# Optimization experiments

Hardware: AMD Instinct MI355X
Metric: run time of the kernel (lower is better)

Reference implementation:

```python
import jax, jax.numpy as jnp
import numpy as np

N = 50000
F_IN = 256
H1, D1 = 8, 8            # conv1: 8 heads x 8 dims, concat -> 64
H2, C = 8, 16            # conv2: 8 heads x num_classes, concat -> 128
NEG_SLOPE = 0.2


def setup_inputs() -> dict:
    key = jax.random.key(0)
    ks = jax.random.split(key, 10)
    x = jax.random.normal(ks[0], (N, F_IN), dtype=jnp.float32)
    edge_index = jax.random.randint(ks[1], (2, 800000), 0, N, dtype=jnp.int64)
    s1 = 1.0 / np.sqrt(F_IN)
    s2 = 1.0 / np.sqrt(H1 * D1)
    return {
        "x": x,
        "edge_index": edge_index,
        "W1": jax.random.normal(ks[2], (F_IN, H1 * D1), dtype=jnp.float32) * s1,
        "a1_src": jax.random.normal(ks[3], (H1, D1), dtype=jnp.float32) * s2,
        "a1_dst": jax.random.normal(ks[4], (H1, D1), dtype=jnp.float32) * s2,
        "b1": jnp.zeros((H1 * D1,), dtype=jnp.float32),
        "W2": jax.random.normal(ks[5], (H1 * D1, H2 * C), dtype=jnp.float32) * s2,
        "a2_src": jax.random.normal(ks[6], (H2, C), dtype=jnp.float32) * (1.0 / np.sqrt(C)),
        "a2_dst": jax.random.normal(ks[7], (H2, C), dtype=jnp.float32) * (1.0 / np.sqrt(C)),
        "b2": jnp.zeros((H2 * C,), dtype=jnp.float32),
    }


def _add_self_loops(edge_index, n):
    loops = jnp.arange(n, dtype=edge_index.dtype)
    return jnp.concatenate([edge_index, jnp.stack([loops, loops])], axis=1)


def _gat_conv(x, src, dst, W, a_src, a_dst, b, heads, out_dim, n):
    # xw: [N, H, O]
    xw = (x @ W).reshape(n, heads, out_dim)
    al_src = jnp.einsum("nho,ho->nh", xw, a_src)  # [N, H]
    al_dst = jnp.einsum("nho,ho->nh", xw, a_dst)
    e = jax.nn.leaky_relu(al_src[src] + al_dst[dst], NEG_SLOPE)  # [E, H]
    # segment softmax over edges sharing a destination node
    e_max = jax.ops.segment_max(e, dst, num_segments=n)
    e_exp = jnp.exp(e - e_max[dst])
    denom = jax.ops.segment_sum(e_exp, dst, num_segments=n)
    alpha = e_exp / (denom[dst] + 1e-16)                          # [E, H]
    msg = xw[src] * alpha[:, :, None]                              # [E, H, O]
    out = jax.ops.segment_sum(msg, dst, num_segments=n)           # [N, H, O]
    return out.reshape(n, heads * out_dim) + b, alpha


def reference(x, edge_index, W1, a1_src, a1_dst, b1, W2, a2_src, a2_dst, b2):
    ei = _add_self_loops(edge_index, N)
    src, dst = ei[0], ei[1]
    # dropout is a no-op at inference (training=False)
    h1, alpha1 = _gat_conv(x, src, dst, W1, a1_src, a1_dst, b1, H1, D1, N)
    h1 = jax.nn.elu(h1)
    h2, _ = _gat_conv(h1, src, dst, W2, a2_src, a2_dst, b2, H2, C, N)
    logp = jax.nn.log_softmax(h2, axis=1)
    return logp, alpha1
```

## Files before the change

### kernel.cpp

```cpp
#include <hip/hip_runtime.h>

#define N_NODES 50000
#define N_EDGES 800000
#define N_TOT   850000
#define NEG 0.2f
#define ELLW 64

#define G1_TILES 391
#define G2_TILES 782

#define NBIN   250
#define NPBIN  200
#define BKBLK  200
#define EPBK   4000
#define BCAP   32
#define OCAP   4096

__device__ __forceinline__ float leaky(float x) { return x > 0.f ? x : NEG * x; }

__device__ __forceinline__ unsigned bf16pk(float a, float b) {
  unsigned ua = __float_as_uint(a), ub = __float_as_uint(b);
  ua = (ua + 0x7FFFu + ((ua >> 16) & 1u)) >> 16;
  ub = (ub + 0x7FFFu + ((ub >> 16) & 1u)) >> 16;
  return ua | (ub << 16);
}
__device__ __forceinline__ float blo(unsigned u) { return __uint_as_float(u << 16); }
__device__ __forceinline__ float bhi(unsigned u) { return __uint_as_float(u & 0xFFFF0000u); }
__device__ __forceinline__ float bh2f(unsigned short h) { return __uint_as_float(((unsigned)h) << 16); }

__global__ __launch_bounds__(256) void bin_gemm1_k(const float* __restrict__ x,
    const float* __restrict__ W1, const float* __restrict__ a1sv, const float* __restrict__ a1dv,
    unsigned short* __restrict__ xw1h, float* __restrict__ al1s, float* __restrict__ a1dd,
    const int* __restrict__ srcA, const int* __restrict__ dstA,
    unsigned* __restrict__ slots, unsigned short* __restrict__ bcnt2,
    unsigned* __restrict__ ofl, int* __restrict__ ofc)
{
  __shared__ __align__(16) char smem[33024];
  const int t = threadIdx.x;
  if (blockIdx.x < BKBLK) {
    unsigned (*buf)[BCAP] = (unsigned(*)[BCAP])smem;
    int* bc = (int*)(smem + 32000);
    for (int k = t; k < NBIN; k += 256) bc[k] = 0;
    __syncthreads();
    const int e0 = blockIdx.x * EPBK;
#pragma unroll
    for (int j = 0; j < 4; ++j) {
      int i4 = j * 256 + t;
      if (i4 < EPBK / 4) {
        int4 s4 = ((const int4*)(srcA + e0))[i4];
        int4 d4 = ((const int4*)(dstA + e0))[i4];
        int dd[4] = {d4.x, d4.y, d4.z, d4.w};
        int ss[4] = {s4.x, s4.y, s4.z, s4.w};
#pragma unroll
        for (int q = 0; q < 4; ++q) {
          int bin = dd[q] / NPBIN;
          unsigned rec = (unsigned)dd[q] | ((unsigned)ss[q] << 16);
          int p = atomicAdd(&bc[bin], 1);
          if (p < BCAP) buf[bin][p] = rec;
          else { int g = atomicAdd(ofc, 1); if (g < OCAP) ofl[g] = rec; }
        }
      }
    }
    __syncthreads();
    const int wv = t >> 6, ln = t & 63;
    for (int b = wv; b < NBIN; b += 4) {
      int c = bc[b]; if (c > BCAP) c = BCAP;
      if (ln == 0) bcnt2[(size_t)b * BKBLK + blockIdx.x] = (unsigned short)c;
      if (ln < c) slots[((size_t)b * BKBLK + blockIdx.x) * BCAP + ln] = buf[b][ln];
    }
    return;
  }
  float* xs  = (float*)smem;
  float* wsm = (float*)(smem + 16384);
  const int tx = t & 15, ty = t >> 4;
  const int n0 = (blockIdx.x - BKBLK) * 128;
  const int nl = t >> 1;
  const int ks = (t & 1) * 16;
  const int wk = t >> 3;
  const int wc = (t & 7) * 8;
  int gn = n0 + nl; if (gn >= N_NODES) gn = N_NODES - 1;
  const float* xrowb = x + (size_t)gn * 256 + ks;

  float acc[8][4];
#pragma unroll
  for (int r = 0; r < 8; ++r)
#pragma unroll
    for (int i = 0; i < 4; ++i) acc[r][i] = 0.f;

  float4 xv0, xv1, xv2, xv3, wv0, wv1;
  {
    const float4* xp = (const float4*)xrowb;
    xv0 = xp[0]; xv1 = xp[1]; xv2 = xp[2]; xv3 = xp[3];
    const float* wrow = W1 + (size_t)wk * 64 + wc;
    wv0 = ((const float4*)wrow)[0];
    wv1 = ((const float4*)wrow)[1];
  }
  for (int kc = 0; kc < 8; ++kc) {
    __syncthreads();
    xs[(ks + 0) * 128 + nl] = xv0.x;  xs[(ks + 1) * 128 + nl] = xv0.y;
    xs[(ks + 2) * 128 + nl] = xv0.z;  xs[(ks + 3) * 128 + nl] = xv0.w;
    xs[(ks + 4) * 128 + nl] = xv1.x;  xs[(ks + 5) * 128 + nl] = xv1.y;
    xs[(ks + 6) * 128 + nl] = xv1.z;  xs[(ks + 7) * 128 + nl] = xv1.w;
    xs[(ks + 8) * 128 + nl] = xv2.x;  xs[(ks + 9) * 128 + nl] = xv2.y;
    xs[(ks + 10) * 128 + nl] = xv2.z; xs[(ks + 11) * 128 + nl] = xv2.w;
    xs[(ks + 12) * 128 + nl] = xv3.x; xs[(ks + 13) * 128 + nl] = xv3.y;
    xs[(ks + 14) * 128 + nl] = xv3.z; xs[(ks + 15) * 128 + nl] = xv3.w;
    ((float4*)&wsm[wk * 64 + wc])[0] = wv0;
    ((float4*)&wsm[wk * 64 + wc])[1] = wv1;
    __syncthreads();
    if (kc < 7) {
      const int kb = (kc + 1) * 32;
      const float4* xp = (const float4*)(xrowb + kb);
      xv0 = xp[0]; xv1 = xp[1]; xv2 = xp[2]; xv3 = xp[3];
      const float* wrow = W1 + (size_t)(kb + wk) * 64 + wc;
      wv0 = ((const float4*)wrow)[0];
      wv1 = ((const float4*)wrow)[1];
    }
#pragma unroll 4
    for (int k = 0; k < 32; ++k) {
      float4 xa = *(const float4*)&xs[k * 128 + ty * 8];
      float4 xb = *(const float4*)&xs[k * 128 + ty * 8 + 4];
      float4 wv = *(const float4*)&wsm[k * 64 + tx * 4];
      float xn[8]; *(float4*)&xn[0] = xa; *(float4*)&xn[4] = xb;
      float wn[4]; *(float4*)wn = wv;
#pragma unroll
      for (int r = 0; r < 8; ++r)
#pragma unroll
        for (int i = 0; i < 4; ++i) acc[r][i] += xn[r] * wn[i];
    }
  }
  float cs[4], cd[4];
#pragma unroll
  for (int i = 0; i < 4; ++i) { cs[i] = a1sv[tx * 4 + i]; cd[i] = a1dv[tx * 4 + i]; }
#pragma unroll
  for (int r = 0; r < 8; ++r) {
    int n = n0 + ty * 8 + r;
    if (n >= N_NODES) break;
    uint2 pk;
    pk.x = bf16pk(acc[r][0], acc[r][1]);
    pk.y = bf16pk(acc[r][2], acc[r][3]);
    *(uint2*)(xw1h + (size_t)n * 64 + tx * 4) = pk;
    float ps = acc[r][0] * cs[0] + acc[r][1] * cs[1] + acc[r][2] * cs[2] + acc[r][3] * cs[3];
    float pd = acc[r][0] * cd[0] + acc[r][1] * cd[1] + acc[r][2] * cd[2] + acc[r][3] * cd[3];
    ps += __shfl_xor(ps, 1);
    pd += __shfl_xor(pd, 1);
    if ((tx & 1) == 0) {
      al1s[n * 8 + (tx >> 1)] = ps;
      a1dd[n * 16 + (tx >> 1)] = pd;
    }
  }
}

__global__ __launch_bounds__(256) void ell_k(const unsigned* __restrict__ slots,
    const unsigned short* __restrict__ bcnt2, const unsigned* __restrict__ ofl,
    const int* __restrict__ ofc, int* __restrict__ cnt, unsigned short* __restrict__ ell)
{
  __shared__ unsigned short ell_lds[NPBIN * ELLW];
  __shared__ int cnt_lds[NPBIN];
  const int t = threadIdx.x;
  const int b = blockIdx.x;
  for (int k = t; k < NPBIN; k += 256) cnt_lds[k] = 0;
  __syncthreads();
  if (t < BKBLK) {
    int c = bcnt2[(size_t)b * BKBLK + t];
    const uint4* sp4 = (const uint4*)(slots + ((size_t)b * BKBLK + t) * BCAP);
    uint4 R[8];
#pragma unroll
    for (int q = 0; q < 8; ++q) R[q] = sp4[q];
#pragma unroll
    for (int j = 0; j < BCAP; ++j) {
      if (j < c) {
        unsigned rec = ((const unsigned*)R)[j];
        int row = (int)(rec & 0xFFFFu) - b * NPBIN;
        int p = atomicAdd(&cnt_lds[row], 1);
        if (p < ELLW) ell_lds[row * ELLW + p] = (unsigned short)(rec >> 16);
      }
    }
  }
  __syncthreads();
  int oc = *ofc; if (oc > OCAP) oc = OCAP;
  for (int i = t; i < oc; i += 256) {
    unsigned rec = ofl[i];
    int d = rec & 0xFFFFu;
    if (d >= b * NPBIN && d < (b + 1) * NPBIN) {
      int p = atomicAdd(&cnt_lds[d - b * NPBIN], 1);
      if (p < ELLW) ell_lds[(d - b * NPBIN) * ELLW + p] = (unsigned short)(rec >> 16);
    }
  }
  __syncthreads();
  const uint4* s4 = (const uint4*)ell_lds;
  uint4* d4 = (uint4*)(ell + (size_t)b * NPBIN * ELLW);
  for (int i = t; i < NPBIN * ELLW / 8; i += 256) d4[i] = s4[i];
  for (int k = t; k < NPBIN; k += 256) cnt[b * NPBIN + k] = cnt_lds[k];
}

__global__ __launch_bounds__(256) void agg1_k(const unsigned short* __restrict__ xw1h,
    const float* __restrict__ al1s, float* __restrict__ a1dd,
    const int* __restrict__ cnt, const unsigned short* __restrict__ ell,
    const float* __restrict__ b1, float* __restrict__ h1)
{
  const int lane = threadIdx.x & 63;
  const int n = blockIdx.x * 4 + (threadIdx.x >> 6);
  if (n >= N_NODES) return;
  const int h = lane >> 3;
  const float ad = a1dd[n * 16 + h];
  float ws = __expf(leaky(al1s[n * 8 + h] + ad));
  float den0 = ws, den1r = 0.f;
  float acc0 = ws * bh2f(xw1h[(size_t)n * 64 + lane]), acc1 = 0.f;
  int num = cnt[n]; if (num > ELLW) num = ELLW;
  const uint4* cp = (const uint4*)(ell + (size_t)n * ELLW);
  int i = 0;
  for (; i + 8 <= num; i += 8) {
    uint4 A = cp[i >> 3];
    int s0 = A.x & 0xFFFF, s1 = (int)(A.x >> 16);
    int s2 = A.y & 0xFFFF, s3 = (int)(A.y >> 16);
    int s4 = A.z & 0xFFFF, s5 = (int)(A.z >> 16);
    int s6 = A.w & 0xFFFF, s7 = (int)(A.w >> 16);
    float l0 = al1s[s0 * 8 + h] + ad, l1 = al1s[s1 * 8 + h] + ad;
    float l2 = al1s[s2 * 8 + h] + ad, l3 = al1s[s3 * 8 + h] + ad;
    float l4 = al1s[s4 * 8 + h] + ad, l5 = al1s[s5 * 8 + h] + ad;
    float l6 = al1s[s6 * 8 + h] + ad, l7 = al1s[s7 * 8 + h] + ad;
    float v0 = bh2f(xw1h[(size_t)s0 * 64 + lane]), v1 = bh2f(xw1h[(size_t)s1 * 64 + lane]);
    float v2 = bh2f(xw1h[(size_t)s2 * 64 + lane]), v3 = bh2f(xw1h[(size_t)s3 * 64 + lane]);
    float v4 = bh2f(xw1h[(size_t)s4 * 64 + lane]), v5 = bh2f(xw1h[(size_t)s5 * 64 + lane]);
    float v6 = bh2f(xw1h[(size_t)s6 * 64 + lane]), v7 = bh2f(xw1h[(size_t)s7 * 64 + lane]);
    float w0 = __expf(leaky(l0)), w1 = __expf(leaky(l1));
    float w2 = __expf(leaky(l2)), w3 = __expf(leaky(l3));
    float w4 = __expf(leaky(l4)), w5 = __expf(leaky(l5));
    float w6 = __expf(leaky(l6)), w7 = __expf(leaky(l7));
    acc0 += w0 * v0; acc1 += w1 * v1; acc0 += w2 * v2; acc1 += w3 * v3;
    acc0 += w4 * v4; acc1 += w5 * v5; acc0 += w6 * v6; acc1 += w7 * v7;
    den0 += w0 + w2 + w4 + w6; den1r += w1 + w3 + w5 + w7;
  }
  for (; i + 4 <= num; i += 4) {
    uint2 A = *(const uint2*)(ell + (size_t)n * ELLW + i);
    int s0 = A.x & 0xFFFF, s1 = (int)(A.x >> 16);
    int s2 = A.y & 0xFFFF, s3 = (int)(A.y >> 16);
    float l0 = al1s[s0 * 8 + h] + ad, l1 = al1s[s1 * 8 + h] + ad;
    float l2 = al1s[s2 * 8 + h] + ad, l3 = al1s[s3 * 8 + h] + ad;
    float v0 = bh2f(xw1h[(size_t)s0 * 64 + lane]), v1 = bh2f(xw1h[(size_t)s1 * 64 + lane]);
    float v2 = bh2f(xw1h[(size_t)s2 * 64 + lane]), v3 = bh2f(xw1h[(size_t)s3 * 64 + lane]);
    float w0 = __expf(leaky(l0)), w1 = __expf(leaky(l1));
    float w2 = __expf(leaky(l2)), w3 = __expf(leaky(l3));
    acc0 += w0 * v0; acc1 += w1 * v1; acc0 += w2 * v2; acc1 += w3 * v3;
    den0 += w0 + w2; den1r += w1 + w3;
  }
  for (; i < num; ++i) {
    int s = ell[(size_t)n * ELLW + i];
    float w = __expf(leaky(al1s[s * 8 + h] + ad));
    acc0 += w * bh2f(xw1h[(size_t)s * 64 + lane]);
    den0 += w;
  }
  float den = den0 + den1r, acc = acc0 + acc1;
  if ((lane & 7) == 0) a1dd[n * 16 + 8 + h] = den;
  float o = acc / (den + 1e-16f) + b1[lane];
  h1[(size_t)n * 64 + lane] = o > 0.f ? o : (__expf(o) - 1.f);
}

__global__ __launch_bounds__(256) void gemm2_alpha_k(const float* __restrict__ h1,
    const float* __restrict__ W2, const float* __restrict__ a2sv, const float* __restrict__ a2dv,
    unsigned* __restrict__ xw2b, float* __restrict__ al2s, float* __restrict__ al2d,
    const int* __restrict__ srcA, const int* __restrict__ dstA,
    const float* __restrict__ al1s, const float* __restrict__ a1dd,
    float* __restrict__ alpha_out)
{
  __shared__ float xs[64 * 64];
  __shared__ float wsm[64 * 128];
  if (blockIdx.x >= G2_TILES) {
    int e = (blockIdx.x - G2_TILES) * 256 + threadIdx.x;
    if (e >= N_TOT) return;
    int s, d;
    if (e < N_EDGES) { s = srcA[e]; d = dstA[e]; }
    else             { s = d = e - N_EDGES; }
    float4 as0 = ((const float4*)(al1s + s * 8))[0];
    float4 as1 = ((const float4*)(al1s + s * 8))[1];
    const float4* dd = (const float4*)(a1dd + d * 16);
    float4 ad0 = dd[0];
    float4 ad1 = dd[1];
    float4 dn0 = dd[2];
    float4 dn1 = dd[3];
    float4 o0, o1;
    o0.x = __expf(leaky(as0.x + ad0.x)) / (dn0.x + 1e-16f);
    o0.y = __expf(leaky(as0.y + ad0.y)) / (dn0.y + 1e-16f);
    o0.z = __expf(leaky(as0.z + ad0.z)) / (dn0.z + 1e-16f);
    o0.w = __expf(leaky(as0.w + ad0.w)) / (dn0.w + 1e-16f);
    o1.x = __expf(leaky(as1.x + ad1.x)) / (dn1.x + 1e-16f);
    o1.y = __expf(leaky(as1.y + ad1.y)) / (dn1.y + 1e-16f);
    o1.z = __expf(leaky(as1.z + ad1.z)) / (dn1.z + 1e-16f);
    o1.w = __expf(leaky(as1.w + ad1.w)) / (dn1.w + 1e-16f);
    ((float4*)(alpha_out + (size_t)e * 8))[0] = o0;
    ((float4*)(alpha_out + (size_t)e * 8))[1] = o1;
    return;
  }
  const int t = threadIdx.x;
  const int tx = t & 15, ty = t >> 4;
  const int n0 = blockIdx.x * 64;
  {
    const int nl = t >> 2;
    const int ks = (t & 3) * 16;
    int gn = n0 + nl; if (gn >= N_NODES) gn = N_NODES - 1;
    const float4* hp = (const float4*)(h1 + (size_t)gn * 64 + ks);
#pragma unroll
    for (int j = 0; j < 4; ++j) {
      float4 v = hp[j];
      xs[(ks + 4 * j + 0) * 64 + nl] = v.x;
      xs[(ks + 4 * j + 1) * 64 + nl] = v.y;
      xs[(ks + 4 * j + 2) * 64 + nl] = v.z;
      xs[(ks + 4 * j + 3) * 64 + nl] = v.w;
    }
    const int wk = t >> 2;
    const int wc = (t & 3) * 32;
    const float4* wp = (const float4*)(W2 + (size_t)wk * 128 + wc);
    float4* wd = (float4*)&wsm[wk * 128 + wc];
#pragma unroll
    for (int j = 0; j < 8; ++j) wd[j] = wp[j];
  }
  __syncthreads();
  float acc[4][8];
#pragma unroll
  for (int r = 0; r < 4; ++r)
#pragma unroll
    for (int i = 0; i < 8; ++i) acc[r][i] = 0.f;
#pragma unroll 4
  for (int k = 0; k < 64; ++k) {
    float4 xa = *(const float4*)&xs[k * 64 + ty * 4];
    float4 wa = *(const float4*)&wsm[k * 128 + tx * 8];
    float4 wb = *(const float4*)&wsm[k * 128 + tx * 8 + 4];
    float xn[4]; *(float4*)xn = xa;
    float wn[8]; *(float4*)&wn[0] = wa; *(float4*)&wn[4] = wb;
#pragma unroll
    for (int r = 0; r < 4; ++r)
#pragma unroll
      for (int i = 0; i < 8; ++i) acc[r][i] += xn[r] * wn[i];
  }
  float cs[8], cd[8];
#pragma unroll
  for (int i = 0; i < 8; ++i) { cs[i] = a2sv[tx * 8 + i]; cd[i] = a2dv[tx * 8 + i]; }
#pragma unroll
  for (int r = 0; r < 4; ++r) {
    int n = n0 + ty * 4 + r;
    if (n >= N_NODES) break;
    uint4 pk;
    pk.x = bf16pk(acc[r][0], acc[r][1]);
    pk.y = bf16pk(acc[r][2], acc[r][3]);
    pk.z = bf16pk(acc[r][4], acc[r][5]);
    pk.w = bf16pk(acc[r][6], acc[r][7]);
    *(uint4*)(xw2b + (size_t)n * 64 + tx * 4) = pk;
    float ps = 0.f, pd = 0.f;
#pragma unroll
    for (int i = 0; i < 8; ++i) { ps += acc[r][i] * cs[i]; pd += acc[r][i] * cd[i]; }
    ps += __shfl_xor(ps, 1);
    pd += __shfl_xor(pd, 1);
    if ((tx & 1) == 0) {
      al2s[n * 8 + (tx >> 1)] = ps;
      al2d[n * 8 + (tx >> 1)] = pd;
    }
  }
}

__global__ __launch_bounds__(256) void agg2_k(const unsigned* __restrict__ xw2b,
    const float* __restrict__ al2s, const float* __restrict__ al2d,
    const int* __restrict__ cnt, const unsigned short* __restrict__ ell,
    const float* __restrict__ b2, float* __restrict__ logp)
{
  const int lane = threadIdx.x & 63;
  const int n = blockIdx.x * 4 + (threadIdx.x >> 6);
  if (n >= N_NODES) return;
  const int h = lane >> 3;
  const float ad = al2d[n * 8 + h];
  float ws = __expf(leaky(al2s[n * 8 + h] + ad));
  unsigned su = xw2b[(size_t)n * 64 + lane];
  float den0 = ws, den1r = 0.f;
  float ax0 = ws * blo(su), ay0 = ws * bhi(su), ax1 = 0.f, ay1 = 0.f;
  int num = cnt[n]; if (num > ELLW) num = ELLW;
  const uint4* cp = (const uint4*)(ell + (size_t)n * ELLW);
  int i = 0;
  for (; i + 8 <= num; i += 8) {
    uint4 A = cp[i >> 3];
    int s0 = A.x & 0xFFFF, s1 = (int)(A.x >> 16);
    int s2 = A.y & 0xFFFF, s3 = (int)(A.y >> 16);
    int s4 = A.z & 0xFFFF, s5 = (int)(A.z >> 16);
    int s6 = A.w & 0xFFFF, s7 = (int)(A.w >> 16);
    float l0 = al2s[s0 * 8 + h] + ad, l1 = al2s[s1 * 8 + h] + ad;
    float l2 = al2s[s2 * 8 + h] + ad, l3 = al2s[s3 * 8 + h] + ad;
    float l4 = al2s[s4 * 8 + h] + ad, l5 = al2s[s5 * 8 + h] + ad;
    float l6 = al2s[s6 * 8 + h] + ad, l7 = al2s[s7 * 8 + h] + ad;
    unsigned u0 = xw2b[(size_t)s0 * 64 + lane], u1 = xw2b[(size_t)s1 * 64 + lane];
    unsigned u2 = xw2b[(size_t)s2 * 64 + lane], u3 = xw2b[(size_t)s3 * 64 + lane];
    unsigned u4 = xw2b[(size_t)s4 * 64 + lane], u5 = xw2b[(size_t)s5 * 64 + lane];
    unsigned u6 = xw2b[(size_t)s6 * 64 + lane], u7 = xw2b[(size_t)s7 * 64 + lane];
    float w0 = __expf(leaky(l0)), w1 = __expf(leaky(l1));
    float w2 = __expf(leaky(l2)), w3 = __expf(leaky(l3));
    float w4 = __expf(leaky(l4)), w5 = __expf(leaky(l5));
    float w6 = __expf(leaky(l6)), w7 = __expf(leaky(l7));
    ax0 += w0 * blo(u0); ay0 += w0 * bhi(u0);
    ax1 += w1 * blo(u1); ay1 += w1 * bhi(u1);
    ax0 += w2 * blo(u2); ay0 += w2 * bhi(u2);
    ax1 += w3 * blo(u3); ay1 += w3 * bhi(u3);
    ax0 += w4 * blo(u4); ay0 += w4 * bhi(u4);
    ax1 += w5 * blo(u5); ay1 += w5 * bhi(u5);
    ax0 += w6 * blo(u6); ay0 += w6 * bhi(u6);
    ax1 += w7 * blo(u7); ay1 += w7 * bhi(u7);
    den0 += w0 + w2 + w4 + w6; den1r += w1 + w3 + w5 + w7;
  }
  for (; i + 4 <= num; i += 4) {
    uint2 A = *(const uint2*)(ell + (size_t)n * ELLW + i);
    int s0 = A.x & 0xFFFF, s1 = (int)(A.x >> 16);
    int s2 = A.y & 0xFFFF, s3 = (int)(A.y >> 16);
    float l0 = al2s[s0 * 8 + h] + ad, l1 = al2s[s1 * 8 + h] + ad;
    float l2 = al2s[s2 * 8 + h] + ad, l3 = al2s[s3 * 8 + h] + ad;
    unsigned u0 = xw2b[(size_t)s0 * 64 + lane], u1 = xw2b[(size_t)s1 * 64 + lane];
    unsigned u2 = xw2b[(size_t)s2 * 64 + lane], u3 = xw2b[(size_t)s3 * 64 + lane];
    float w0 = __expf(leaky(l0)), w1 = __expf(leaky(l1));
    float w2 = __expf(leaky(l2)), w3 = __expf(leaky(l3));
    ax0 += w0 * blo(u0); ay0 += w0 * bhi(u0);
    ax1 += w1 * blo(u1); ay1 += w1 * bhi(u1);
    ax0 += w2 * blo(u2); ay0 += w2 * bhi(u2);
    ax1 += w3 * blo(u3); ay1 += w3 * bhi(u3);
    den0 += w0 + w2; den1r += w1 + w3;
  }
  for (; i < num; ++i) {
    int s = ell[(size_t)n * ELLW + i];
    float w = __expf(leaky(al2s[s * 8 + h] + ad));
    unsigned u = xw2b[(size_t)s * 64 + lane];
    ax0 += w * blo(u); ay0 += w * bhi(u); den0 += w;
  }
  float inv = 1.f / (den0 + den1r + 1e-16f);
  float o0 = (ax0 + ax1) * inv + b2[2 * lane];
  float o1 = (ay0 + ay1) * inv + b2[2 * lane + 1];
  float mx = fmaxf(o0, o1);
#pragma unroll
  for (int off = 1; off < 64; off <<= 1) mx = fmaxf(mx, __shfl_xor(mx, off));
  float se = __expf(o0 - mx) + __expf(o1 - mx);
#pragma unroll
  for (int off = 1; off < 64; off <<= 1) se += __shfl_xor(se, off);
  float lse = mx + __logf(se);
  float2 o; o.x = o0 - lse; o.y = o1 - lse;
  ((float2*)logp)[(size_t)n * 64 + lane] = o;
}

extern "C" void kernel_launch(void* const* d_in, const int* in_sizes, int n_in,
                              void* d_out, int out_size, void* d_ws, size_t ws_size,
                              hipStream_t stream)
{
  const float* x   = (const float*)d_in[0];
  const int*   ei  = (const int*)d_in[1];
  const float* W1  = (const float*)d_in[2];
  const float* a1s = (const float*)d_in[3];
  const float* a1d = (const float*)d_in[4];
  const float* b1  = (const float*)d_in[5];
  const float* W2  = (const float*)d_in[6];
  const float* a2s = (const float*)d_in[7];
  const float* a2d = (const float*)d_in[8];
  const float* b2  = (const float*)d_in[9];
  const int* srcA = ei;
  const int* dstA = ei + N_EDGES;

  char* ws = (char*)d_ws;
  unsigned short* xw1h = (unsigned short*)ws;            ws += (size_t)N_NODES * 64 * 2;
  float* h1    = (float*)ws;  ws += (size_t)N_NODES * 64 * 4;
  unsigned* xw2b = (unsigned*)ws; ws += (size_t)N_NODES * 64 * 4;
  float* al1s_ = (float*)ws;  ws += (size_t)N_NODES * 8 * 4;
  float* a1dd_ = (float*)ws;  ws += (size_t)N_NODES * 16 * 4;
  float* al2s_ = (float*)ws;  ws += (size_t)N_NODES * 8 * 4;
  float* al2d_ = (float*)ws;  ws += (size_t)N_NODES * 8 * 4;
  int* cnt    = (int*)ws;     ws += (size_t)N_NODES * 4;
  unsigned short* ell = (unsigned short*)ws; ws += (size_t)N_NODES * ELLW * 2;
  unsigned* slots = (unsigned*)ws; ws += (size_t)NBIN * BKBLK * BCAP * 4;
  unsigned short* bcnt2 = (unsigned short*)ws; ws += (size_t)NBIN * BKBLK * 2;
  unsigned* ofl = (unsigned*)ws; ws += (size_t)OCAP * 4;
  int* ofc = (int*)ws; ws += 16;

  float* logp      = (float*)d_out;
  float* alpha_out = logp + (size_t)N_NODES * 128;

  hipMemsetAsync(ofc, 0, sizeof(int), stream);

  bin_gemm1_k<<<BKBLK + G1_TILES, 256, 0, stream>>>(
      x, W1, a1s, a1d, xw1h, al1s_, a1dd_, srcA, dstA, slots, bcnt2, ofl, ofc);
  ell_k<<<NBIN, 256, 0, stream>>>(slots, bcnt2, ofl, ofc, cnt, ell);
  agg1_k<<<(N_NODES + 3) / 4, 256, 0, stream>>>(xw1h, al1s_, a1dd_, cnt, ell, b1, h1);
  gemm2_alpha_k<<<G2_TILES + (N_TOT + 255) / 256, 256, 0, stream>>>(
      h1, W2, a2s, a2d, xw2b, al2s_, al2d_, srcA, dstA, al1s_, a1dd_, alpha_out);
  agg2_k<<<(N_NODES + 3) / 4, 256, 0, stream>>>(xw2b, al2s_, al2d_, cnt, ell, b2, logp);
}
```

Baseline: 158.9 us.

## Distribute edge attention logits across lanes and shrink GEMM1 tiles to 64 rows

The two aggregation kernels now have each lane compute one (edge, head) attention weight per group of 8 edges, so each of the 8 exps runs once instead of being repeated by every lane of a head. Weights and source indices are broadcast to the other lanes with shuffles. This removes redundant exp and logit loads but adds shuffle traffic and drops the 4-edge unrolled tail. Separately, the first projection GEMM uses 64-node tiles with 4x4 per-thread accumulators, doubling the tile count to raise parallelism at the cost of less register reuse.

```diff
diff --git a/kernel.cpp b/kernel.cpp
--- a/kernel.cpp
+++ b/kernel.cpp
@@ -6,7 +6,7 @@
 #define NEG 0.2f
 #define ELLW 64
 
-#define G1_TILES 391
+#define G1_TILES 782
 #define G2_TILES 782
 
 #define NBIN   250
@@ -71,60 +71,55 @@
     return;
   }
   float* xs  = (float*)smem;
-  float* wsm = (float*)(smem + 16384);
+  float* wsm = (float*)(smem + 8192);
   const int tx = t & 15, ty = t >> 4;
-  const int n0 = (blockIdx.x - BKBLK) * 128;
-  const int nl = t >> 1;
-  const int ks = (t & 1) * 16;
+  const int n0 = (blockIdx.x - BKBLK) * 64;
+  const int nl = t >> 2;
+  const int ks = (t & 3) * 8;
   const int wk = t >> 3;
   const int wc = (t & 7) * 8;
   int gn = n0 + nl; if (gn >= N_NODES) gn = N_NODES - 1;
   const float* xrowb = x + (size_t)gn * 256 + ks;
 
-  float acc[8][4];
-#pragma unroll
-  for (int r = 0; r < 8; ++r)
+  float acc[4][4];
+#pragma unroll
+  for (int r = 0; r < 4; ++r)
 #pragma unroll
     for (int i = 0; i < 4; ++i) acc[r][i] = 0.f;
 
-  float4 xv0, xv1, xv2, xv3, wv0, wv1;
+  float4 xv0, xv1, wv0, wv1;
   {
     const float4* xp = (const float4*)xrowb;
-    xv0 = xp[0]; xv1 = xp[1]; xv2 = xp[2]; xv3 = xp[3];
+    xv0 = xp[0]; xv1 = xp[1];
     const float* wrow = W1 + (size_t)wk * 64 + wc;
     wv0 = ((const float4*)wrow)[0];
     wv1 = ((const float4*)wrow)[1];
   }
   for (int kc = 0; kc < 8; ++kc) {
     __syncthreads();
-    xs[(ks + 0) * 128 + nl] = xv0.x;  xs[(ks + 1) * 128 + nl] = xv0.y;
-    xs[(ks + 2) * 128 + nl] = xv0.z;  xs[(ks + 3) * 128 + nl] = xv0.w;
-    xs[(ks + 4) * 128 + nl] = xv1.x;  xs[(ks + 5) * 128 + nl] = xv1.y;
-    xs[(ks + 6) * 128 + nl] = xv1.z;  xs[(ks + 7) * 128 + nl] = xv1.w;
-    xs[(ks + 8) * 128 + nl] = xv2.x;  xs[(ks + 9) * 128 + nl] = xv2.y;
-    xs[(ks + 10) * 128 + nl] = xv2.z; xs[(ks + 11) * 128 + nl] = xv2.w;
-    xs[(ks + 12) * 128 + nl] = xv3.x; xs[(ks + 13) * 128 + nl] = xv3.y;
-    xs[(ks + 14) * 128 + nl] = xv3.z; xs[(ks + 15) * 128 + nl] = xv3.w;
+    xs[(ks + 0) * 64 + nl] = xv0.x;  xs[(ks + 1) * 64 + nl] = xv0.y;
+    xs[(ks + 2) * 64 + nl] = xv0.z;  xs[(ks + 3) * 64 + nl] = xv0.w;
+    xs[(ks + 4) * 64 + nl] = xv1.x;  xs[(ks + 5) * 64 + nl] = xv1.y;
+    xs[(ks + 6) * 64 + nl] = xv1.z;  xs[(ks + 7) * 64 + nl] = xv1.w;
     ((float4*)&wsm[wk * 64 + wc])[0] = wv0;
     ((float4*)&wsm[wk * 64 + wc])[1] = wv1;
     __syncthreads();
     if (kc < 7) {
       const int kb = (kc + 1) * 32;
       const float4* xp = (const float4*)(xrowb + kb);
-      xv0 = xp[0]; xv1 = xp[1]; xv2 = xp[2]; xv3 = xp[3];
+      xv0 = xp[0]; xv1 = xp[1];
       const float* wrow = W1 + (size_t)(kb + wk) * 64 + wc;
       wv0 = ((const float4*)wrow)[0];
       wv1 = ((const float4*)wrow)[1];
     }
 #pragma unroll 4
     for (int k = 0; k < 32; ++k) {
-      float4 xa = *(const float4*)&xs[k * 128 + ty * 8];
-      float4 xb = *(const float4*)&xs[k * 128 + ty * 8 + 4];
+      float4 xa = *(const float4*)&xs[k * 64 + ty * 4];
       float4 wv = *(const float4*)&wsm[k * 64 + tx * 4];
-      float xn[8]; *(float4*)&xn[0] = xa; *(float4*)&xn[4] = xb;
+      float xn[4]; *(float4*)xn = xa;
       float wn[4]; *(float4*)wn = wv;
 #pragma unroll
-      for (int r = 0; r < 8; ++r)
+      for (int r = 0; r < 4; ++r)
 #pragma unroll
         for (int i = 0; i < 4; ++i) acc[r][i] += xn[r] * wn[i];
     }
@@ -133,8 +128,8 @@
 #pragma unroll
   for (int i = 0; i < 4; ++i) { cs[i] = a1sv[tx * 4 + i]; cd[i] = a1dv[tx * 4 + i]; }
 #pragma unroll
-  for (int r = 0; r < 8; ++r) {
-    int n = n0 + ty * 8 + r;
+  for (int r = 0; r < 4; ++r) {
+    int n = n0 + ty * 4 + r;
     if (n >= N_NODES) break;
     uint2 pk;
     pk.x = bf16pk(acc[r][0], acc[r][1]);
@@ -203,55 +198,35 @@
   const int n = blockIdx.x * 4 + (threadIdx.x >> 6);
   if (n >= N_NODES) return;
   const int h = lane >> 3;
+  const int hw = lane & 7;
+  const int ew = lane >> 3;
   const float ad = a1dd[n * 16 + h];
+  const float adH = __shfl(ad, hw << 3);
   float ws = __expf(leaky(al1s[n * 8 + h] + ad));
-  float den0 = ws, den1r = 0.f;
+  float den0 = ws, den1 = 0.f;
   float acc0 = ws * bh2f(xw1h[(size_t)n * 64 + lane]), acc1 = 0.f;
   int num = cnt[n]; if (num > ELLW) num = ELLW;
-  const uint4* cp = (const uint4*)(ell + (size_t)n * ELLW);
+  const unsigned short* erow = ell + (size_t)n * ELLW;
   int i = 0;
   for (; i + 8 <= num; i += 8) {
-    uint4 A = cp[i >> 3];
-    int s0 = A.x & 0xFFFF, s1 = (int)(A.x >> 16);
-    int s2 = A.y & 0xFFFF, s3 = (int)(A.y >> 16);
-    int s4 = A.z & 0xFFFF, s5 = (int)(A.z >> 16);
-    int s6 = A.w & 0xFFFF, s7 = (int)(A.w >> 16);
-    float l0 = al1s[s0 * 8 + h] + ad, l1 = al1s[s1 * 8 + h] + ad;
-    float l2 = al1s[s2 * 8 + h] + ad, l3 = al1s[s3 * 8 + h] + ad;
-    float l4 = al1s[s4 * 8 + h] + ad, l5 = al1s[s5 * 8 + h] + ad;
-    float l6 = al1s[s6 * 8 + h] + ad, l7 = al1s[s7 * 8 + h] + ad;
-    float v0 = bh2f(xw1h[(size_t)s0 * 64 + lane]), v1 = bh2f(xw1h[(size_t)s1 * 64 + lane]);
-    float v2 = bh2f(xw1h[(size_t)s2 * 64 + lane]), v3 = bh2f(xw1h[(size_t)s3 * 64 + lane]);
-    float v4 = bh2f(xw1h[(size_t)s4 * 64 + lane]), v5 = bh2f(xw1h[(size_t)s5 * 64 + lane]);
-    float v6 = bh2f(xw1h[(size_t)s6 * 64 + lane]), v7 = bh2f(xw1h[(size_t)s7 * 64 + lane]);
-    float w0 = __expf(leaky(l0)), w1 = __expf(leaky(l1));
-    float w2 = __expf(leaky(l2)), w3 = __expf(leaky(l3));
-    float w4 = __expf(leaky(l4)), w5 = __expf(leaky(l5));
-    float w6 = __expf(leaky(l6)), w7 = __expf(leaky(l7));
-    acc0 += w0 * v0; acc1 += w1 * v1; acc0 += w2 * v2; acc1 += w3 * v3;
-    acc0 += w4 * v4; acc1 += w5 * v5; acc0 += w6 * v6; acc1 += w7 * v7;
-    den0 += w0 + w2 + w4 + w6; den1r += w1 + w3 + w5 + w7;
-  }
-  for (; i + 4 <= num; i += 4) {
-    uint2 A = *(const uint2*)(ell + (size_t)n * ELLW + i);
-    int s0 = A.x & 0xFFFF, s1 = (int)(A.x >> 16);
-    int s2 = A.y & 0xFFFF, s3 = (int)(A.y >> 16);
-    float l0 = al1s[s0 * 8 + h] + ad, l1 = al1s[s1 * 8 + h] + ad;
-    float l2 = al1s[s2 * 8 + h] + ad, l3 = al1s[s3 * 8 + h] + ad;
-    float v0 = bh2f(xw1h[(size_t)s0 * 64 + lane]), v1 = bh2f(xw1h[(size_t)s1 * 64 + lane]);
-    float v2 = bh2f(xw1h[(size_t)s2 * 64 + lane]), v3 = bh2f(xw1h[(size_t)s3 * 64 + lane]);
-    float w0 = __expf(leaky(l0)), w1 = __expf(leaky(l1));
-    float w2 = __expf(leaky(l2)), w3 = __expf(leaky(l3));
-    acc0 += w0 * v0; acc1 += w1 * v1; acc0 += w2 * v2; acc1 += w3 * v3;
-    den0 += w0 + w2; den1r += w1 + w3;
+    int sw = erow[i + ew];
+    float wv = __expf(leaky(al1s[sw * 8 + hw] + adH));
+#pragma unroll
+    for (int j = 0; j < 8; ++j) {
+      int sj = __shfl(sw, j << 3);
+      float wj = __shfl(wv, (j << 3) + h);
+      float vj = bh2f(xw1h[(size_t)sj * 64 + lane]);
+      if (j & 1) { acc1 += wj * vj; den1 += wj; }
+      else       { acc0 += wj * vj; den0 += wj; }
+    }
   }
   for (; i < num; ++i) {
-    int s = ell[(size_t)n * ELLW + i];
+    int s = erow[i];
     float w = __expf(leaky(al1s[s * 8 + h] + ad));
     acc0 += w * bh2f(xw1h[(size_t)s * 64 + lane]);
     den0 += w;
   }
-  float den = den0 + den1r, acc = acc0 + acc1;
+  float den = den0 + den1, acc = acc0 + acc1;
   if ((lane & 7) == 0) a1dd[n * 16 + 8 + h] = den;
   float o = acc / (den + 1e-16f) + b1[lane];
   h1[(size_t)n * 64 + lane] = o > 0.f ? o : (__expf(o) - 1.f);
@@ -367,65 +342,36 @@
   const int n = blockIdx.x * 4 + (threadIdx.x >> 6);
   if (n >= N_NODES) return;
   const int h = lane >> 3;
+  const int hw = lane & 7;
+  const int ew = lane >> 3;
   const float ad = al2d[n * 8 + h];
+  const float adH = __shfl(ad, hw << 3);
   float ws = __expf(leaky(al2s[n * 8 + h] + ad));
   unsigned su = xw2b[(size_t)n * 64 + lane];
-  float den0 = ws, den1r = 0.f;
+  float den0 = ws, den1 = 0.f;
   float ax0 = ws * blo(su), ay0 = ws * bhi(su), ax1 = 0.f, ay1 = 0.f;
   int num = cnt[n]; if (num > ELLW) num = ELLW;
-  const uint4* cp = (const uint4*)(ell + (size_t)n * ELLW);
+  const unsigned short* erow = ell + (size_t)n * ELLW;
   int i = 0;
   for (; i + 8 <= num; i += 8) {
-    uint4 A = cp[i >> 3];
-    int s0 = A.x & 0xFFFF, s1 = (int)(A.x >> 16);
-    int s2 = A.y & 0xFFFF, s3 = (int)(A.y >> 16);
-    int s4 = A.z & 0xFFFF, s5 = (int)(A.z >> 16);
-    int s6 = A.w & 0xFFFF, s7 = (int)(A.w >> 16);
-    float l0 = al2s[s0 * 8 + h] + ad, l1 = al2s[s1 * 8 + h] + ad;
-    float l2 = al2s[s2 * 8 + h] + ad, l3 = al2s[s3 * 8 + h] + ad;
-    float l4 = al2s[s4 * 8 + h] + ad, l5 = al2s[s5 * 8 + h] + ad;
-    float l6 = al2s[s6 * 8 + h] + ad, l7 = al2s[s7 * 8 + h] + ad;
-    unsigned u0 = xw2b[(size_t)s0 * 64 + lane], u1 = xw2b[(size_t)s1 * 64 + lane];
-    unsigned u2 = xw2b[(size_t)s2 * 64 + lane], u3 = xw2b[(size_t)s3 * 64 + lane];
-    unsigned u4 = xw2b[(size_t)s4 * 64 + lane], u5 = xw2b[(size_t)s5 * 64 + lane];
-    unsigned u6 = xw2b[(size_t)s6 * 64 + lane], u7 = xw2b[(size_t)s7 * 64 + lane];
-    float w0 = __expf(leaky(l0)), w1 = __expf(leaky(l1));
-    float w2 = __expf(leaky(l2)), w3 = __expf(leaky(l3));
-    float w4 = __expf(leaky(l4)), w5 = __expf(leaky(l5));
-    float w6 = __expf(leaky(l6)), w7 = __expf(leaky(l7));
-    ax0 += w0 * blo(u0); ay0 += w0 * bhi(u0);
-    ax1 += w1 * blo(u1); ay1 += w1 * bhi(u1);
-    ax0 += w2 * blo(u2); ay0 += w2 * bhi(u2);
-    ax1 += w3 * blo(u3); ay1 += w3 * bhi(u3);
-    ax0 += w4 * blo(u4); ay0 += w4 * bhi(u4);
-    ax1 += w5 * blo(u5); ay1 += w5 * bhi(u5);
-    ax0 += w6 * blo(u6); ay0 += w6 * bhi(u6);
-    ax1 += w7 * blo(u7); ay1 += w7 * bhi(u7);
-    den0 += w0 + w2 + w4 + w6; den1r += w1 + w3 + w5 + w7;
-  }
-  for (; i + 4 <= num; i += 4) {
-    uint2 A = *(const uint2*)(ell + (size_t)n * ELLW + i);
-    int s0 = A.x & 0xFFFF, s1 = (int)(A.x >> 16);
-    int s2 = A.y & 0xFFFF, s3 = (int)(A.y >> 16);
-    float l0 = al2s[s0 * 8 + h] + ad, l1 = al2s[s1 * 8 + h] + ad;
-    float l2 = al2s[s2 * 8 + h] + ad, l3 = al2s[s3 * 8 + h] + ad;
-    unsigned u0 = xw2b[(size_t)s0 * 64 + lane], u1 = xw2b[(size_t)s1 * 64 + lane];
-    unsigned u2 = xw2b[(size_t)s2 * 64 + lane], u3 = xw2b[(size_t)s3 * 64 + lane];
-    float w0 = __expf(leaky(l0)), w1 = __expf(leaky(l1));
-    float w2 = __expf(leaky(l2)), w3 = __expf(leaky(l3));
-    ax0 += w0 * blo(u0); ay0 += w0 * bhi(u0);
-    ax1 += w1 * blo(u1); ay1 += w1 * bhi(u1);
-    ax0 += w2 * blo(u2); ay0 += w2 * bhi(u2);
-    ax1 += w3 * blo(u3); ay1 += w3 * bhi(u3);
-    den0 += w0 + w2; den1r += w1 + w3;
+    int sw = erow[i + ew];
+    float wv = __expf(leaky(al2s[sw * 8 + hw] + adH));
+#pragma unroll
+    for (int j = 0; j < 8; ++j) {
+      int sj = __shfl(sw, j << 3);
+      float wj = __shfl(wv, (j << 3) + h);
+      unsigned u = xw2b[(size_t)sj * 64 + lane];
+      if (j & 1) { ax1 += wj * blo(u); ay1 += wj * bhi(u); den1 += wj; }
+      else       { ax0 += wj * blo(u); ay0 += wj * bhi(u); den0 += wj; }
+    }
   }
   for (; i < num; ++i) {
-    int s = ell[(size_t)n * ELLW + i];
+    int s = erow[i];
     float w = __expf(leaky(al2s[s * 8 + h] + ad));
     unsigned u = xw2b[(size_t)s * 64 + lane];
     ax0 += w * blo(u); ay0 += w * bhi(u); den0 += w;
   }
-  float inv = 1.f / (den0 + den1r + 1e-16f);
+  float inv = 1.f / (den0 + den1 + 1e-16f);
   float o0 = (ax0 + ax1) * inv + b2[2 * lane];
   float o1 = (ay0 + ay1) * inv + b2[2 * lane + 1];
   float mx = fmaxf(o0, o1);
```

After: 172.0 us. 8.2% more time.

## Shrink GEMM1 tiles to 32 rows and split edge binning into two LDS passes

Applied to the files above, without the earlier changes.

The fused binning+GEMM1 kernel cuts its shared memory footprint roughly in half. The binning blocks now process their destination bins in two halves, re-reading the edge chunk each pass, so the buffer only needs 125 bins. The GEMM blocks use 32-node tiles with a 2x4 register micro-tile instead of 128-node tiles with 8x4, quadrupling the tile count. This raises occupancy and parallelism but lowers per-thread arithmetic reuse and doubles the edge reads in binning.

```diff
diff --git a/kernel.cpp b/kernel.cpp
--- a/kernel.cpp
+++ b/kernel.cpp
@@ -6,7 +6,7 @@
 #define NEG 0.2f
 #define ELLW 64
 
-#define G1_TILES 391
+#define G1_TILES 1563
 #define G2_TILES 782
 
 #define NBIN   250
@@ -15,6 +15,7 @@
 #define EPBK   4000
 #define BCAP   32
 #define OCAP   4096
+#define HBIN   125
 
 __device__ __forceinline__ float leaky(float x) { return x > 0.f ? x : NEG * x; }
 
@@ -35,106 +36,103 @@
     unsigned* __restrict__ slots, unsigned short* __restrict__ bcnt2,
     unsigned* __restrict__ ofl, int* __restrict__ ofc)
 {
-  __shared__ __align__(16) char smem[33024];
+  __shared__ __align__(16) char smem[16512];
   const int t = threadIdx.x;
   if (blockIdx.x < BKBLK) {
     unsigned (*buf)[BCAP] = (unsigned(*)[BCAP])smem;
-    int* bc = (int*)(smem + 32000);
-    for (int k = t; k < NBIN; k += 256) bc[k] = 0;
-    __syncthreads();
+    int* bc = (int*)(smem + 16000);
     const int e0 = blockIdx.x * EPBK;
-#pragma unroll
-    for (int j = 0; j < 4; ++j) {
-      int i4 = j * 256 + t;
-      if (i4 < EPBK / 4) {
-        int4 s4 = ((const int4*)(srcA + e0))[i4];
-        int4 d4 = ((const int4*)(dstA + e0))[i4];
-        int dd[4] = {d4.x, d4.y, d4.z, d4.w};
-        int ss[4] = {s4.x, s4.y, s4.z, s4.w};
-#pragma unroll
-        for (int q = 0; q < 4; ++q) {
-          int bin = dd[q] / NPBIN;
-          unsigned rec = (unsigned)dd[q] | ((unsigned)ss[q] << 16);
-          int p = atomicAdd(&bc[bin], 1);
-          if (p < BCAP) buf[bin][p] = rec;
-          else { int g = atomicAdd(ofc, 1); if (g < OCAP) ofl[g] = rec; }
+    for (int pass = 0; pass < 2; ++pass) {
+      const int b_lo = pass * HBIN;
+      for (int k = t; k < HBIN; k += 256) bc[k] = 0;
+      __syncthreads();
+#pragma unroll
+      for (int j = 0; j < 4; ++j) {
+        int i4 = j * 256 + t;
+        if (i4 < EPBK / 4) {
+          int4 s4 = ((const int4*)(srcA + e0))[i4];
+          int4 d4 = ((const int4*)(dstA + e0))[i4];
+          int dd[4] = {d4.x, d4.y, d4.z, d4.w};
+          int ss[4] = {s4.x, s4.y, s4.z, s4.w};
+#pragma unroll
+          for (int q = 0; q < 4; ++q) {
+            int bin = dd[q] / NPBIN - b_lo;
+            if ((unsigned)bin < HBIN) {
+              unsigned rec = (unsigned)dd[q] | ((unsigned)ss[q] << 16);
+              int p = atomicAdd(&bc[bin], 1);
+              if (p < BCAP) buf[bin][p] = rec;
+              else { int g = atomicAdd(ofc, 1); if (g < OCAP) ofl[g] = rec; }
+            }
+          }
         }
       }
-    }
-    __syncthreads();
-    const int wv = t >> 6, ln = t & 63;
-    for (int b = wv; b < NBIN; b += 4) {
-      int c = bc[b]; if (c > BCAP) c = BCAP;
-      if (ln == 0) bcnt2[(size_t)b * BKBLK + blockIdx.x] = (unsigned short)c;
-      if (ln < c) slots[((size_t)b * BKBLK + blockIdx.x) * BCAP + ln] = buf[b][ln];
+      __syncthreads();
+      const int wv = t >> 6, ln = t & 63;
+      for (int b = wv; b < HBIN; b += 4) {
+        int c = bc[b]; if (c > BCAP) c = BCAP;
+        int gb = b_lo + b;
+        if (ln == 0) bcnt2[(size_t)gb * BKBLK + blockIdx.x] = (unsigned short)c;
+        if (ln < c) slots[((size_t)gb * BKBLK + blockIdx.x) * BCAP + ln] = buf[b][ln];
+      }
+      __syncthreads();
     }
     return;
   }
   float* xs  = (float*)smem;
-  float* wsm = (float*)(smem + 16384);
+  float* wsm = (float*)(smem + 4352);
   const int tx = t & 15, ty = t >> 4;
-  const int n0 = (blockIdx.x - BKBLK) * 128;
-  const int nl = t >> 1;
-  const int ks = (t & 1) * 16;
+  const int n0 = (blockIdx.x - BKBLK) * 32;
+  const int xrow = t >> 3;
+  const int xc   = (t & 7) * 4;
   const int wk = t >> 3;
   const int wc = (t & 7) * 8;
-  int gn = n0 + nl; if (gn >= N_NODES) gn = N_NODES - 1;
-  const float* xrowb = x + (size_t)gn * 256 + ks;
-
-  float acc[8][4];
-#pragma unroll
-  for (int r = 0; r < 8; ++r)
+  int gn = n0 + xrow; if (gn >= N_NODES) gn = N_NODES - 1;
+  const float* xrowb = x + (size_t)gn * 256 + xc;
+
+  float acc[2][4];
+#pragma unroll
+  for (int r = 0; r < 2; ++r)
 #pragma unroll
     for (int i = 0; i < 4; ++i) acc[r][i] = 0.f;
 
-  float4 xv0, xv1, xv2, xv3, wv0, wv1;
-  {
-    const float4* xp = (const float4*)xrowb;
-    xv0 = xp[0]; xv1 = xp[1]; xv2 = xp[2]; xv3 = xp[3];
-    const float* wrow = W1 + (size_t)wk * 64 + wc;
-    wv0 = ((const float4*)wrow)[0];
-    wv1 = ((const float4*)wrow)[1];
-  }
+  float4 xv, wv0, wv1;
+  xv  = *(const float4*)xrowb;
+  wv0 = ((const float4*)(W1 + (size_t)wk * 64 + wc))[0];
+  wv1 = ((const float4*)(W1 + (size_t)wk * 64 + wc))[1];
   for (int kc = 0; kc < 8; ++kc) {
     __syncthreads();
-    xs[(ks + 0) * 128 + nl] = xv0.x;  xs[(ks + 1) * 128 + nl] = xv0.y;
-    xs[(ks + 2) * 128 + nl] = xv0.z;  xs[(ks + 3) * 128 + nl] = xv0.w;
-    xs[(ks + 4) * 128 + nl] = xv1.x;  xs[(ks + 5) * 128 + nl] = xv1.y;
-    xs[(ks + 6) * 128 + nl] = xv1.z;  xs[(ks + 7) * 128 + nl] = xv1.w;
-    xs[(ks + 8) * 128 + nl] = xv2.x;  xs[(ks + 9) * 128 + nl] = xv2.y;
-    xs[(ks + 10) * 128 + nl] = xv2.z; xs[(ks + 11) * 128 + nl] = xv2.w;
-    xs[(ks + 12) * 128 + nl] = xv3.x; xs[(ks + 13) * 128 + nl] = xv3.y;
-    xs[(ks + 14) * 128 + nl] = xv3.z; xs[(ks + 15) * 128 + nl] = xv3.w;
+    xs[(xc + 0) * 34 + xrow] = xv.x;
+    xs[(xc + 1) * 34 + xrow] = xv.y;
+    xs[(xc + 2) * 34 + xrow] = xv.z;
+    xs[(xc + 3) * 34 + xrow] = xv.w;
     ((float4*)&wsm[wk * 64 + wc])[0] = wv0;
     ((float4*)&wsm[wk * 64 + wc])[1] = wv1;
     __syncthreads();
     if (kc < 7) {
       const int kb = (kc + 1) * 32;
-      const float4* xp = (const float4*)(xrowb + kb);
-      xv0 = xp[0]; xv1 = xp[1]; xv2 = xp[2]; xv3 = xp[3];
+      xv  = *(const float4*)(xrowb + kb);
       const float* wrow = W1 + (size_t)(kb + wk) * 64 + wc;
       wv0 = ((const float4*)wrow)[0];
       wv1 = ((const float4*)wrow)[1];
     }
-#pragma unroll 4
+#pragma unroll 8
     for (int k = 0; k < 32; ++k) {
-      float4 xa = *(const float4*)&xs[k * 128 + ty * 8];
-      float4 xb = *(const float4*)&xs[k * 128 + ty * 8 + 4];
+      float2 xa = *(const float2*)&xs[k * 34 + ty * 2];
       float4 wv = *(const float4*)&wsm[k * 64 + tx * 4];
-      float xn[8]; *(float4*)&xn[0] = xa; *(float4*)&xn[4] = xb;
       float wn[4]; *(float4*)wn = wv;
 #pragma unroll
-      for (int r = 0; r < 8; ++r)
-#pragma unroll
-        for (int i = 0; i < 4; ++i) acc[r][i] += xn[r] * wn[i];
+      for (int i = 0; i < 4; ++i) {
+        acc[0][i] += xa.x * wn[i];
+        acc[1][i] += xa.y * wn[i];
+      }
     }
   }
   float cs[4], cd[4];
 #pragma unroll
   for (int i = 0; i < 4; ++i) { cs[i] = a1sv[tx * 4 + i]; cd[i] = a1dv[tx * 4 + i]; }
 #pragma unroll
-  for (int r = 0; r < 8; ++r) {
-    int n = n0 + ty * 8 + r;
+  for (int r = 0; r < 2; ++r) {
+    int n = n0 + ty * 2 + r;
     if (n >= N_NODES) break;
     uint2 pk;
     pk.x = bf16pk(acc[r][0], acc[r][1]);
```

Measured after the change: 163.0 us. 1.03x slower.
